# Kernel optimization log

Measured on AMD Instinct MI355X. Metric: run time of the kernel, lower is better.

## Reference

```python
import jax, jax.numpy as jnp
import numpy as np

C = 3.0
K = 1.0 / C
SQRT_K = K ** 0.5
GAMMA = 0.1
LAMBDA_STRUCTURE = 5.0
EPS = 1e-7
MIN_NORM = 1e-15
MAX_SQDIST = 50.0

N_NODES = 100000
HID = 64
E_POS = 250000
E_NEG = 250000
E_NONE = E_POS + E_NEG


def _arcosh(x):
    return jnp.log(x + jnp.sqrt(x * x - 1.0))


def hyp_sqdist(x, y):
    # Minkowski inner product: <x,y>_L = sum(x*y) - 2*x0*y0
    mdot = jnp.sum(x * y, axis=-1) - 2.0 * x[..., 0] * y[..., 0]
    theta = jnp.maximum(-mdot / K, 1.0 + EPS)
    return jnp.minimum(K * _arcosh(theta) ** 2, MAX_SQDIST)


def hyp_proj(x):
    # project onto hyperboloid: x0 = sqrt(K + ||x_1:||^2)
    y = x[..., 1:]
    x0 = jnp.sqrt(K + jnp.sum(y * y, axis=-1, keepdims=True))
    return jnp.concatenate([x0, y], axis=-1)


def hyp_expmap0(u):
    x = u[..., 1:]
    xn = jnp.maximum(jnp.sqrt(jnp.sum(x * x, axis=-1, keepdims=True)), MIN_NORM)
    theta = xn / SQRT_K
    res = jnp.concatenate([SQRT_K * jnp.cosh(theta), SQRT_K * jnp.sinh(theta) * x / xn], axis=-1)
    return hyp_proj(res)


def discriminate(z, ei, lin_w, lin_b):
    v = jnp.concatenate([z[ei[0]], z[ei[1]]], axis=-1)  # [E, 2*HID]
    return jax.nn.log_softmax(v @ lin_w.T + lin_b, axis=-1)


def info_net(v, y, w1, b1, w2, b2):
    # MINE-style critic: concat(edge_feature, label) -> Linear -> ReLU -> Linear -> scalar
    h = jnp.concatenate([v, y[:, None]], axis=-1)
    h = jax.nn.relu(h @ w1.T + b1)
    return (h @ w2.T + b2)[:, 0]


def setup_inputs():
    key = jax.random.key(0)
    ks = jax.random.split(key, 16)
    z = jax.random.normal(ks[0], (N_NODES, HID), dtype=jnp.float32)
    lin_w = 0.05 * jax.random.normal(ks[1], (3, 2 * HID), dtype=jnp.float32)
    lin_b = jnp.zeros((3,), dtype=jnp.float32)
    d_info = 2 * (HID + 1)
    info_w1 = 0.02 * jax.random.normal(ks[2], (d_info, d_info + 1), dtype=jnp.float32)
    info_b1 = jnp.zeros((d_info,), dtype=jnp.float32)
    info_w2 = 0.02 * jax.random.normal(ks[3], (1, d_info), dtype=jnp.float32)
    info_b2 = jnp.zeros((1,), dtype=jnp.float32)
    pos_edge_index = jax.random.randint(ks[4], (2, E_POS), 0, N_NODES)
    neg_edge_index = jax.random.randint(ks[5], (2, E_NEG), 0, N_NODES)
    none_edge_index = jax.random.randint(ks[6], (2, E_NONE), 0, N_NODES)
    none_edge_index2 = jax.random.randint(ks[7], (2, E_NONE), 0, N_NODES)
    pos_k = jax.random.randint(ks[8], (E_POS,), 0, N_NODES)
    neg_k = jax.random.randint(ks[9], (E_NEG,), 0, N_NODES)
    perm = jax.random.permutation(ks[10], E_POS + E_NEG + E_NONE)
    return dict(z=z, lin_w=lin_w, lin_b=lin_b, info_w1=info_w1, info_b1=info_b1,
                info_w2=info_w2, info_b2=info_b2, pos_edge_index=pos_edge_index,
                neg_edge_index=neg_edge_index, none_edge_index=none_edge_index,
                none_edge_index2=none_edge_index2, pos_k=pos_k, neg_k=neg_k, perm=perm)


def reference(z, lin_w, lin_b, info_w1, info_b1, info_w2, info_b2,
              pos_edge_index, neg_edge_index, none_edge_index,
              none_edge_index2, pos_k, neg_k, perm):
    # lift z onto the hyperboloid: proj(expmap0(proj_tan0([z0 | z])))
    vals = jnp.concatenate([z[:, :1], z], axis=1)      # [N, HID+1]
    u = vals.at[:, 0].set(0.0)                          # proj_tan0
    x = hyp_proj(hyp_expmap0(u))                        # [N, HID+1]

    # nll discriminator loss (class targets 0 / 1 / 2)
    nll = (jnp.mean(-discriminate(z, pos_edge_index, lin_w, lin_b)[:, 0])
           + jnp.mean(-discriminate(z, neg_edge_index, lin_w, lin_b)[:, 1])
           + jnp.mean(-discriminate(z, none_edge_index, lin_w, lin_b)[:, 2])) / 3.0

    # structured triplet losses on the hyperboloid
    i, j = pos_edge_index[0], pos_edge_index[1]
    l1 = jnp.mean(jnp.maximum(hyp_sqdist(x[i], x[j]) - hyp_sqdist(x[i], x[pos_k]), 0.0))
    i, j = neg_edge_index[0], neg_edge_index[1]
    l2 = jnp.mean(jnp.maximum(hyp_sqdist(x[i], x[neg_k]) - hyp_sqdist(x[i], x[j]), 0.0))

    # mutual-information (MINE) term on hyperbolic embeddings
    idx = jnp.concatenate([pos_edge_index, neg_edge_index, none_edge_index2], axis=1)
    all_y = jnp.concatenate([
        jnp.zeros((pos_edge_index.shape[1],), jnp.float32),
        jnp.ones((neg_edge_index.shape[1],), jnp.float32),
        jnp.full((none_edge_index2.shape[1],), 2.0, jnp.float32)])
    value = jnp.concatenate([x[idx[0]], x[idx[1]]], axis=1)  # [E_all, 2*(HID+1)]
    info_pred = info_net(value, all_y, info_w1, info_b1, info_w2, info_b2)
    info_shuffle = info_net(value, all_y[perm], info_w1, info_b1, info_w2, info_b2)
    l3 = -(jnp.mean(info_pred) - jnp.log(jnp.mean(jnp.exp(info_shuffle))))

    return nll + LAMBDA_STRUCTURE * (l1 + l2) + GAMMA * l3
```

## Files before the change

kernel.cpp:

```cpp
#include <hip/hip_runtime.h>
#include <hip/hip_fp16.h>
#include <math.h>

#define NN    100000
#define EPOS  250000
#define ENEG  250000
#define ENON  500000
#define E3   1000000
#define EHALF 500000
#define NLSE  4096

#define NB_INFO   2816
#define NB_STRUCT 960
#define NB_NLL    320
#define NB_EDGES  (NB_INFO + NB_STRUCT + NB_NLL)

#define ACC_OFF 0
#define LSE_OFF 256
#define X0_OFF  66048
#define ZA_OFF  466176
#define ZB_OFF  2066176
#define WT_OFF  3666176
#define YF8_OFF 3722752
#define PT_OFF  10122752
#define QT_OFF  10322752
#define PM_OFF  10522752
#define QM_OFF  23322752

typedef __attribute__((ext_vector_type(8))) short bh8;
typedef __attribute__((ext_vector_type(4))) float f32x4;
typedef __attribute__((ext_vector_type(2))) float f32x2;


__device__ __forceinline__ unsigned short f2bf(float f) {
  unsigned u = __float_as_uint(f);
  unsigned r = (u + 0x7FFFu + ((u >> 16) & 1u)) >> 16;
  return (unsigned short)r;
}

#if __has_builtin(__builtin_amdgcn_cvt_pk_f32_bf8) && __has_builtin(__builtin_amdgcn_cvt_pk_bf8_f32)
#define HAVE_BF8 1
#endif

__device__ __forceinline__ void de4(unsigned v, float* o) {
#ifdef HAVE_BF8
  f32x2 lo = __builtin_amdgcn_cvt_pk_f32_bf8((int)v, false);
  f32x2 hi = __builtin_amdgcn_cvt_pk_f32_bf8((int)v, true);
  o[0] = lo[0]; o[1] = lo[1]; o[2] = hi[0]; o[3] = hi[1];
#else
  o[0] = __half2float(__ushort_as_half((unsigned short)((v & 0xFFu) << 8)));
  o[1] = __half2float(__ushort_as_half((unsigned short)(((v >> 8) & 0xFFu) << 8)));
  o[2] = __half2float(__ushort_as_half((unsigned short)(((v >> 16) & 0xFFu) << 8)));
  o[3] = __half2float(__ushort_as_half((unsigned short)((v >> 24) << 8)));
#endif
}

__device__ __forceinline__ unsigned pk2(float a, float b) {
  a = fminf(fmaxf(a, -57344.f), 57344.f);
  b = fminf(fmaxf(b, -57344.f), 57344.f);
#ifdef HAVE_BF8
  return (unsigned)__builtin_amdgcn_cvt_pk_bf8_f32(a, b, 0, false) & 0xFFFFu;
#else
  unsigned short ha = __half_as_ushort(__float2half(a));
  unsigned short hb = __half_as_ushort(__float2half(b));
  ha = (unsigned short)((ha + 0x7Fu + ((ha >> 8) & 1u)) >> 8);
  hb = (unsigned short)((hb + 0x7Fu + ((hb >> 8) & 1u)) >> 8);
  return (unsigned)ha | ((unsigned)hb << 8);
#endif
}

__device__ __forceinline__ void breduce2(double v0, double v1, double* g0, double* g1,
                                         double* rbuf) {
#pragma unroll
  for (int m = 32; m; m >>= 1) {
    v0 += __shfl_xor(v0, m, 64);
    v1 += __shfl_xor(v1, m, 64);
  }
  int l = threadIdx.x & 63, w = threadIdx.x >> 6;
  if (l == 0) { rbuf[2 * w] = v0; rbuf[2 * w + 1] = v1; }
  __syncthreads();
  if (threadIdx.x == 0) {
    int nw = blockDim.x >> 6;
    double s0 = 0.0, s1 = 0.0;
    for (int i = 0; i < nw; ++i) { s0 += rbuf[2 * i]; s1 += rbuf[2 * i + 1]; }
    atomicAdd(g0, s0);
    atomicAdd(g1, s1);
  }
}

__device__ __forceinline__ void lse_combine(double& m, double& s, double om, double os) {
  double M = fmax(m, om);
  double sn = 0.0;
  if (m > -INFINITY) sn += s * exp(m - M);
  if (om > -INFINITY) sn += os * exp(om - M);
  m = M;
  s = sn;
}

__device__ __forceinline__ void lse_block_reduce(double lm, double ls, double* out_pair,
                                                 double* rbuf) {
#pragma unroll
  for (int d = 32; d; d >>= 1) {
    double om = __shfl_xor(lm, d, 64);
    double os = __shfl_xor(ls, d, 64);
    lse_combine(lm, ls, om, os);
  }
  __syncthreads();
  int l = threadIdx.x & 63, w = threadIdx.x >> 6;
  if (l == 0) { rbuf[2 * w] = lm; rbuf[2 * w + 1] = ls; }
  __syncthreads();
  if (threadIdx.x == 0) {
    int nw = blockDim.x >> 6;
    double M = rbuf[0], S = rbuf[1];
    for (int i = 1; i < nw; ++i) lse_combine(M, S, rbuf[2 * i], rbuf[2 * i + 1]);
    out_pair[0] = M;
    out_pair[1] = S;
  }
}

__global__ __launch_bounds__(256) void k_init(const float* __restrict__ w1,
                                              double* __restrict__ acc,
                                              double* __restrict__ lse,
                                              unsigned short* __restrict__ wt) {
  int gid = blockIdx.x * 256 + threadIdx.x;
  if (gid < NLSE) { lse[2 * gid] = -INFINITY; lse[2 * gid + 1] = 0.0; }
  if (gid < 8) acc[gid] = 0.0;
  for (int u = threadIdx.x; u < 16 * 104; u += 256) {
    int c = 16 * blockIdx.x + u / 104;
    int k = u % 104;
    float val = 0.f;
    if (c < 130) {
      if (k < 64) val = w1[c * 131 + 1 + k];
      else if (k == 64) val = w1[c * 131];
    } else if (c >= 136 && c < 266) {
      int r = c - 136;
      if (k < 64) val = w1[r * 131 + 66 + k];
      else if (k == 64) val = w1[r * 131 + 65];
    }
    wt[(size_t)c * 104 + k] = f2bf(val);
  }
}

__global__ __launch_bounds__(128) void k_pre(
    const float* __restrict__ z, const float* __restrict__ lin_w,
    const unsigned short* __restrict__ wt,
    float* __restrict__ X0, unsigned char* __restrict__ YF8,
    float4* __restrict__ ZA4, float4* __restrict__ ZB4,
    unsigned char* __restrict__ Pm, unsigned char* __restrict__ Qm,
    unsigned char* __restrict__ PTb, unsigned char* __restrict__ QTb) {
  __shared__ float WL[384];
  __shared__ __align__(16) unsigned short YL[128 * 96];
  __shared__ __align__(16) unsigned char SB[2][16 * 304];
  for (int u = threadIdx.x; u < 384; u += 128) {
    int rr = u >> 6, d = u & 63;
    WL[u] = (rr < 3) ? lin_w[rr * 128 + d] : lin_w[(rr - 3) * 128 + 64 + d];
  }
  __syncthreads();
  const int base = blockIdx.x * 128;
  const int n = base + threadIdx.x;
  if (n < NN) {
    const float4* zr = (const float4*)(z + (size_t)n * 64);
    const float4* wl4 = (const float4*)WL;
    float4 zc[16];
    float zn2 = 0.f, d0 = 0.f, d1 = 0.f, d2 = 0.f, d3 = 0.f, d4 = 0.f, d5 = 0.f;
#pragma unroll
    for (int c = 0; c < 16; ++c) {
      float4 v = zr[c];
      zc[c] = v;
      zn2 += v.x * v.x + v.y * v.y + v.z * v.z + v.w * v.w;
      float4 w0 = wl4[c];
      float4 w1r = wl4[16 + c];
      float4 w2r = wl4[32 + c];
      float4 w3 = wl4[48 + c];
      float4 w4 = wl4[64 + c];
      float4 w5 = wl4[80 + c];
      d0 += v.x * w0.x + v.y * w0.y + v.z * w0.z + v.w * w0.w;
      d1 += v.x * w1r.x + v.y * w1r.y + v.z * w1r.z + v.w * w1r.w;
      d2 += v.x * w2r.x + v.y * w2r.y + v.z * w2r.z + v.w * w2r.w;
      d3 += v.x * w3.x + v.y * w3.y + v.z * w3.z + v.w * w3.w;
      d4 += v.x * w4.x + v.y * w4.y + v.z * w4.z + v.w * w4.w;
      d5 += v.x * w5.x + v.y * w5.y + v.z * w5.z + v.w * w5.w;
    }
    float zn = fmaxf(sqrtf(zn2), 1e-15f);
    float t = 1.7320508075688772f * zn;
    float e = __expf(t);
    float sh = 0.5f * (e - __frcp_rn(e));
    float fac = (t < 1e-4f) ? (1.f + t * t * 0.16666667f) : (sh / t);
    float yn2 = fac * fac * zn2;
    float x0 = sqrtf(0.33333333333333333f + yn2);
    X0[n] = x0;
    ZA4[n] = make_float4(d0, d1, d2, 0.f);
    ZB4[n] = make_float4(d3, d4, d5, 0.f);
    unsigned short* yrow = YL + threadIdx.x * 96;
    unsigned yu[16];
#pragma unroll
    for (int c = 0; c < 16; ++c) {
      float4 v = zc[c];
      ushort4 o;
      o.x = f2bf(fac * v.x); o.y = f2bf(fac * v.y);
      o.z = f2bf(fac * v.z); o.w = f2bf(fac * v.w);
      *(ushort4*)(yrow + 4 * c) = o;
      yu[c] = pk2(fac * v.x, fac * v.y) | (pk2(fac * v.z, fac * v.w) << 16);
    }
    ushort4 xx; xx.x = f2bf(x0); xx.y = 0; xx.z = 0; xx.w = 0;
    *(ushort4*)(yrow + 64) = xx;
    ushort4 zz; zz.x = 0; zz.y = 0; zz.z = 0; zz.w = 0;
#pragma unroll
    for (int c = 17; c < 24; ++c) *(ushort4*)(yrow + 4 * c) = zz;
    uint4* y8 = (uint4*)(YF8 + (size_t)n * 64);
    y8[0] = make_uint4(yu[0], yu[1], yu[2], yu[3]);
    y8[1] = make_uint4(yu[4], yu[5], yu[6], yu[7]);
    y8[2] = make_uint4(yu[8], yu[9], yu[10], yu[11]);
    y8[3] = make_uint4(yu[12], yu[13], yu[14], yu[15]);
  }
  __syncthreads();
  const int l = threadIdx.x & 63;
  const int w = threadIdx.x >> 6;
  const int col = l & 15, kq = l >> 4;
  unsigned char* sb = SB[w];
  const int ntiles = min(8, (NN - base) >> 4);
  for (int t = w; t < ntiles; t += 2) {
    const unsigned short* yr = YL + (t * 16 + col) * 96 + kq * 8;
    bh8 y0 = *(const bh8*)(yr);
    bh8 y1 = *(const bh8*)(yr + 32);
    bh8 y2 = *(const bh8*)(yr + 64);
#pragma unroll
    for (int nt = 0; nt < 17; ++nt) {
      const unsigned short* wr = wt + (size_t)(nt * 16 + col) * 104 + kq * 8;
      bh8 b0 = *(const bh8*)(wr);
      bh8 b1 = *(const bh8*)(wr + 32);
      bh8 b2 = *(const bh8*)(wr + 64);
      f32x4 a4 = {0.f, 0.f, 0.f, 0.f};
      a4 = __builtin_amdgcn_mfma_f32_16x16x32_bf16(b0, y0, a4, 0, 0, 0);
      a4 = __builtin_amdgcn_mfma_f32_16x16x32_bf16(b1, y1, a4, 0, 0, 0);
      a4 = __builtin_amdgcn_mfma_f32_16x16x32_bf16(b2, y2, a4, 0, 0, 0);
      int ob = nt * 16 + kq * 4;
      unsigned u = pk2(a4[0], a4[1]) | (pk2(a4[2], a4[3]) << 16);
      unsigned char* row = sb + col * 304;
      if (nt < 8) {
        *(unsigned*)(row + ob) = u;
      } else if (nt == 8) {
        if (kq == 0) *(unsigned short*)(row + 256) = (unsigned short)(u & 0xFFFFu);
        else if (kq >= 2) *(unsigned*)(row + 128 + (ob - 136)) = u;
      } else if (nt < 16) {
        *(unsigned*)(row + 128 + (ob - 136)) = u;
      } else {
        if (kq < 2) *(unsigned*)(row + 128 + (ob - 136)) = u;
        else if (kq == 2) *(unsigned short*)(row + 258) = (unsigned short)(u & 0xFFFFu);
      }
    }
    const size_t gb = (size_t)(base + t * 16);
#pragma unroll
    for (int r = 0; r < 2; ++r) {
      int idx = r * 64 + l;
      int node = idx >> 3, part = idx & 7;
      uint4 vp = *(const uint4*)(sb + node * 304 + part * 16);
      *(uint4*)(Pm + (gb + node) * 128 + part * 16) = vp;
      uint4 vq = *(const uint4*)(sb + node * 304 + 128 + part * 16);
      *(uint4*)(Qm + (gb + node) * 128 + part * 16) = vq;
    }
    if (l < 16) {
      *(unsigned short*)(PTb + (gb + l) * 2) = *(const unsigned short*)(sb + l * 304 + 256);
      *(unsigned short*)(QTb + (gb + l) * 2) = *(const unsigned short*)(sb + l * 304 + 258);
    }
  }
}

__device__ __forceinline__ float hsq(float mdot) {
  float th = fmaxf(-3.f * mdot, 1.f + 1e-7f);
  float ach = __logf(th + sqrtf(th * th - 1.f));
  return fminf(ach * ach * (1.f / 3.f), 50.f);
}

__global__ __launch_bounds__(256) void k_edges(
    const int* __restrict__ p0, const int* __restrict__ p1,
    const int* __restrict__ n0, const int* __restrict__ n1,
    const int* __restrict__ o0, const int* __restrict__ o1,
    const int* __restrict__ q0, const int* __restrict__ q1,
    const int* __restrict__ pk, const int* __restrict__ nk,
    const int* __restrict__ perm,
    const unsigned char* __restrict__ Pm, const unsigned char* __restrict__ Qm,
    const unsigned short* __restrict__ PT, const unsigned short* __restrict__ QT,
    const unsigned char* __restrict__ YF8, const float* __restrict__ X0,
    const float4* __restrict__ ZA4, const float4* __restrict__ ZB4,
    const float* __restrict__ lin_b,
    const float* __restrict__ w1, const float* __restrict__ b1v,
    const float* __restrict__ w2v,
    double* __restrict__ acc, double* __restrict__ lse) {
  __shared__ double rbuf[8];
  __shared__ double rbuf2[8];

  if (blockIdx.x < NB_INFO) {
    const int s8 = threadIdx.x & 7;
    float byr[16], wyr[16], w2r[16];
#pragma unroll
    for (int q = 0; q < 16; ++q) {
      int k = 16 * s8 + q;
      byr[q] = b1v[k];
      wyr[q] = w1[k * 131 + 130];
      w2r[q] = w2v[k];
    }
    const float byt0 = b1v[128], byt1 = b1v[129];
    const float wyt0 = w1[128 * 131 + 130], wyt1 = w1[129 * 131 + 130];
    const float w2t0 = w2v[128], w2t1 = w2v[129];
    int g = (blockIdx.x * 256 + threadIdx.x) >> 3;
    const int gs = (NB_INFO * 256) >> 3;
    float s1f = 0.f, lm = -INFINITY, lsum = 0.f;

    int yAp_c = 0, yAs_c = 0, yBs_c = 0;
    uint4 PA_c = {}, QA_c = {}, PB_c = {}, QB_c = {};
    unsigned ptA_c = 0, qtA_c = 0, ptB_c = 0, qtB_c = 0;

#define FETCH_A(E, YPI, YSI, P4, Q4, PT_, QT_)                                          \
  {                                                                                     \
    int i, j;                                                                           \
    if ((E) < EPOS) { i = p0[E]; j = p1[E]; YPI = 0; }                                  \
    else { int t_ = (E) - EPOS; i = n0[t_]; j = n1[t_]; YPI = 1; }                      \
    int p_ = perm[E];                                                                   \
    YSI = (p_ < EPOS) ? 0 : ((p_ < EPOS + ENEG) ? 1 : 2);                               \
    P4 = *(const uint4*)(Pm + (size_t)i * 128 + 16 * s8);                               \
    Q4 = *(const uint4*)(Qm + (size_t)j * 128 + 16 * s8);                               \
    if (s8 == 0) { PT_ = PT[i]; QT_ = QT[j]; }                                          \
  }
#define FETCH_B(E, YSI, P4, Q4, PT_, QT_)                                               \
  {                                                                                     \
    int i = q0[E], j = q1[E];                                                           \
    int p_ = perm[(E) + EHALF];                                                         \
    YSI = (p_ < EPOS) ? 0 : ((p_ < EPOS + ENEG) ? 1 : 2);                               \
    P4 = *(const uint4*)(Pm + (size_t)i * 128 + 16 * s8);                               \
    Q4 = *(const uint4*)(Qm + (size_t)j * 128 + 16 * s8);                               \
    if (s8 == 0) { PT_ = PT[i]; QT_ = QT[j]; }                                          \
  }
#define INFO_COMPUTE(YPF, YSF, P4, Q4, PT_, QT_)                                        \
  {                                                                                     \
    float pv[16], qv[16];                                                               \
    de4(P4.x, pv); de4(P4.y, pv + 4); de4(P4.z, pv + 8); de4(P4.w, pv + 12);            \
    de4(Q4.x, qv); de4(Q4.y, qv + 4); de4(Q4.z, qv + 8); de4(Q4.w, qv + 12);            \
    float sp = 0.f, ss = 0.f;                                                           \
    _Pragma("unroll") for (int q = 0; q < 16; ++q) {                                    \
      float t_ = pv[q] + qv[q] + byr[q];                                                \
      sp = fmaf(fmaxf(fmaf(YPF, wyr[q], t_), 0.f), w2r[q], sp);                         \
      ss = fmaf(fmaxf(fmaf(YSF, wyr[q], t_), 0.f), w2r[q], ss);                         \
    }                                                                                   \
    if (s8 == 0) {                                                                      \
      float tp[4], tq[4];                                                               \
      de4(PT_, tp); de4(QT_, tq);                                                       \
      float t0 = tp[0] + tq[0] + byt0;                                                  \
      float t1 = tp[1] + tq[1] + byt1;                                                  \
      sp += fmaxf(fmaf(YPF, wyt0, t0), 0.f) * w2t0 + fmaxf(fmaf(YPF, wyt1, t1), 0.f) * w2t1; \
      ss += fmaxf(fmaf(YSF, wyt0, t0), 0.f) * w2t0 + fmaxf(fmaf(YSF, wyt1, t1), 0.f) * w2t1; \
    }                                                                                   \
    _Pragma("unroll") for (int m_ = 4; m_; m_ >>= 1) {                                  \
      sp += __shfl_xor(sp, m_, 64);                                                     \
      ss += __shfl_xor(ss, m_, 64);                                                     \
    }                                                                                   \
    if (s8 == 0) {                                                                      \
      s1f += sp;                                                                        \
      float nm = fmaxf(lm, ss);                                                         \
      lsum = lsum * __expf(lm - nm) + __expf(ss - nm);                                  \
      lm = nm;                                                                          \
    }                                                                                   \
  }

    int e = g;
    if (e < EHALF) {
      FETCH_A(e, yAp_c, yAs_c, PA_c, QA_c, ptA_c, qtA_c);
      FETCH_B(e, yBs_c, PB_c, QB_c, ptB_c, qtB_c);
    }
    while (e < EHALF) {
      int e2 = e + gs;
      int yAp_n = 0, yAs_n = 0, yBs_n = 0;
      uint4 PA_n = {}, QA_n = {}, PB_n = {}, QB_n = {};
      unsigned ptA_n = 0, qtA_n = 0, ptB_n = 0, qtB_n = 0;
      if (e2 < EHALF) {
        FETCH_A(e2, yAp_n, yAs_n, PA_n, QA_n, ptA_n, qtA_n);
        FETCH_B(e2, yBs_n, PB_n, QB_n, ptB_n, qtB_n);
      }
      INFO_COMPUTE((float)yAp_c, (float)yAs_c, PA_c, QA_c, ptA_c, qtA_c);
      INFO_COMPUTE(2.f, (float)yBs_c, PB_c, QB_c, ptB_c, qtB_c);
      e = e2;
      yAp_c = yAp_n; yAs_c = yAs_n; yBs_c = yBs_n;
      PA_c = PA_n; QA_c = QA_n; PB_c = PB_n; QB_c = QB_n;
      ptA_c = ptA_n; qtA_c = qtA_n; ptB_c = ptB_n; qtB_c = qtB_n;
    }
    breduce2((double)s1f, 0.0, acc + 3, acc + 6, rbuf);
    double lmd = (lsum > 0.f) ? (double)lm : -(double)INFINITY;
    lse_block_reduce(lmd, (double)lsum, lse + 2 * blockIdx.x, rbuf2);

  } else if (blockIdx.x < NB_INFO + NB_STRUCT) {
    const int st = threadIdx.x & 7;
    int g = ((blockIdx.x - NB_INFO) * 256 + threadIdx.x) >> 3;
    const int gs = (NB_STRUCT * 256) >> 3;
    float s1f = 0.f, s2f = 0.f;

    bool pos_c = false;
    uint2 yi_c = {}, yj_c = {}, yk_c = {};
    float xi_c = 0.f, xj_c = 0.f, xk_c = 0.f;

#define ST_FETCH(E, POS, YI, YJ, YK, XI, XJ, XK)                       \
  {                                                                    \
    int i, j, kk;                                                      \
    POS = (E) < EPOS;                                                  \
    if (POS) { i = p0[E]; j = p1[E]; kk = pk[E]; }                     \
    else { int t = (E) - EPOS; i = n0[t]; j = n1[t]; kk = nk[t]; }     \
    YI = *(const uint2*)(YF8 + (size_t)i * 64 + 8 * st);               \
    YJ = *(const uint2*)(YF8 + (size_t)j * 64 + 8 * st);               \
    YK = *(const uint2*)(YF8 + (size_t)kk * 64 + 8 * st);              \
    if (st == 0) { XI = X0[i]; XJ = X0[j]; XK = X0[kk]; }              \
  }

    int e = g;
    if (e < EPOS + ENEG) ST_FETCH(e, pos_c, yi_c, yj_c, yk_c, xi_c, xj_c, xk_c);
    while (e < EPOS + ENEG) {
      int e2 = e + gs;
      bool pos_n = false;
      uint2 yi_n = {}, yj_n = {}, yk_n = {};
      float xi_n = 0.f, xj_n = 0.f, xk_n = 0.f;
      if (e2 < EPOS + ENEG) ST_FETCH(e2, pos_n, yi_n, yj_n, yk_n, xi_n, xj_n, xk_n);
      float ai[8], aj[8], ak[8];
      de4(yi_c.x, ai); de4(yi_c.y, ai + 4);
      de4(yj_c.x, aj); de4(yj_c.y, aj + 4);
      de4(yk_c.x, ak); de4(yk_c.y, ak + 4);
      float dij = 0.f, dik = 0.f;
#pragma unroll
      for (int q = 0; q < 8; ++q) {
        dij = fmaf(ai[q], aj[q], dij);
        dik = fmaf(ai[q], ak[q], dik);
      }
#pragma unroll
      for (int m = 4; m; m >>= 1) {
        dij += __shfl_xor(dij, m, 64);
        dik += __shfl_xor(dik, m, 64);
      }
      if (st == 0) {
        float sij = hsq(dij - xi_c * xj_c);
        float sik = hsq(dik - xi_c * xk_c);
        if (pos_c) s1f += fmaxf(sij - sik, 0.f);
        else s2f += fmaxf(sik - sij, 0.f);
      }
      e = e2;
      pos_c = pos_n; yi_c = yi_n; yj_c = yj_n; yk_c = yk_n;
      xi_c = xi_n; xj_c = xj_n; xk_c = xk_n;
    }
    breduce2((double)s1f, (double)s2f, acc + 1, acc + 2, rbuf);

  } else {
    const float c0 = lin_b[0], c1 = lin_b[1], c2 = lin_b[2];
    const float wp = 1.f / (3.f * EPOS), wn = 1.f / (3.f * ENEG), wo = 1.f / (3.f * ENON);
    double s = 0.0;
    int t0 = (blockIdx.x - NB_INFO - NB_STRUCT) * 256 + threadIdx.x;
    for (int e = t0; e < E3; e += NB_NLL * 256) {
      int i, j, tgt;
      float wgt;
      if (e < EPOS) { i = p0[e]; j = p1[e]; tgt = 0; wgt = wp; }
      else if (e < EPOS + ENEG) { int t = e - EPOS; i = n0[t]; j = n1[t]; tgt = 1; wgt = wn; }
      else { int t = e - EPOS - ENEG; i = o0[t]; j = o1[t]; tgt = 2; wgt = wo; }
      float4 a = ZA4[i], b = ZB4[j];
      float l0 = a.x + b.x + c0, l1 = a.y + b.y + c1, l2 = a.z + b.z + c2;
      float mx = fmaxf(l0, fmaxf(l1, l2));
      float lsev = mx + __logf(__expf(l0 - mx) + __expf(l1 - mx) + __expf(l2 - mx));
      float lt = (tgt == 0) ? l0 : ((tgt == 1) ? l1 : l2);
      s += (double)((lsev - lt) * wgt);
    }
    breduce2(s, 0.0, acc + 0, acc + 5, rbuf);
  }
}

__global__ void k_final(const double* __restrict__ acc, const double* __restrict__ lse,
                        float* __restrict__ out) {
  __shared__ double rb[8];
  double lm = -INFINITY, ls = 0.0;
  for (int i = threadIdx.x; i < NLSE; i += blockDim.x)
    lse_combine(lm, ls, lse[2 * i], lse[2 * i + 1]);
#pragma unroll
  for (int d = 32; d; d >>= 1) {
    double om = __shfl_xor(lm, d, 64);
    double os = __shfl_xor(ls, d, 64);
    lse_combine(lm, ls, om, os);
  }
  int l = threadIdx.x & 63, w = threadIdx.x >> 6;
  if (l == 0) { rb[2 * w] = lm; rb[2 * w + 1] = ls; }
  __syncthreads();
  if (threadIdx.x == 0) {
    double M = rb[0], S = rb[1];
    int nw = blockDim.x >> 6;
    for (int i = 1; i < nw; ++i) lse_combine(M, S, rb[2 * i], rb[2 * i + 1]);
    double logmean = M + log(S) - log((double)E3);
    double nll = acc[0];
    double l1 = acc[1] / (double)EPOS;
    double l2 = acc[2] / (double)ENEG;
    double s1m = acc[3] / (double)E3;
    double l3 = -(s1m - logmean);
    out[0] = (float)(nll + 5.0 * (l1 + l2) + 0.1 * l3);
  }
}

extern "C" void kernel_launch(void* const* d_in, const int* in_sizes, int n_in,
                              void* d_out, int out_size, void* d_ws, size_t ws_size,
                              hipStream_t stream) {
  const float* z     = (const float*)d_in[0];
  const float* lin_w = (const float*)d_in[1];
  const float* lin_b = (const float*)d_in[2];
  const float* w1    = (const float*)d_in[3];
  const float* b1v   = (const float*)d_in[4];
  const float* w2v   = (const float*)d_in[5];
  const int* pos  = (const int*)d_in[7];
  const int* neg  = (const int*)d_in[8];
  const int* non  = (const int*)d_in[9];
  const int* non2 = (const int*)d_in[10];
  const int* posk = (const int*)d_in[11];
  const int* negk = (const int*)d_in[12];
  const int* perm = (const int*)d_in[13];

  char* ws = (char*)d_ws;
  double* acc = (double*)(ws + ACC_OFF);
  double* lse = (double*)(ws + LSE_OFF);
  float* X0   = (float*)(ws + X0_OFF);
  float4* ZA4 = (float4*)(ws + ZA_OFF);
  float4* ZB4 = (float4*)(ws + ZB_OFF);
  unsigned short* WT  = (unsigned short*)(ws + WT_OFF);
  unsigned char* YF8  = (unsigned char*)(ws + YF8_OFF);
  unsigned char* PTb  = (unsigned char*)(ws + PT_OFF);
  unsigned char* QTb  = (unsigned char*)(ws + QT_OFF);
  unsigned char* PM   = (unsigned char*)(ws + PM_OFF);
  unsigned char* QM   = (unsigned char*)(ws + QM_OFF);

  hipLaunchKernelGGL(k_init, dim3(17), dim3(256), 0, stream, w1, acc, lse, WT);
  hipLaunchKernelGGL(k_pre, dim3((NN + 127) / 128), dim3(128), 0, stream,
                     z, lin_w, WT, X0, YF8, ZA4, ZB4, PM, QM, PTb, QTb);
  hipLaunchKernelGGL(k_edges, dim3(NB_EDGES), dim3(256), 0, stream,
                     pos, pos + EPOS, neg, neg + ENEG, non, non + ENON,
                     non2, non2 + ENON, posk, negk, perm,
                     PM, QM, (const unsigned short*)PTb, (const unsigned short*)QTb,
                     YF8, X0, ZA4, ZB4, lin_b, w1, b1v, w2v, acc, lse);
  hipLaunchKernelGGL(k_final, dim3(1), dim3(256), 0, stream, acc, lse, (float*)d_out);
}
```

Before: 274.3 us.

## Split node precompute into two kernels and flatten info loop with two-deep prefetch

The fused node-preprocessing kernel is split in two. The first kernel computes the hyperbolic projection and writes bf16 rows to a new global buffer. The second kernel stages the MFMA weight table in shared memory once per block and loops persistently over 16-node tiles, where before every tile re-read the weights from global memory. The info-net edge loop now walks all 1M edges in one flat index space with a two-deep software prefetch instead of processing two halves per iteration. In exchange this adds a ~19MB intermediate write and read plus an extra kernel launch.

```diff
diff --git a/kernel.cpp b/kernel.cpp
--- a/kernel.cpp
+++ b/kernel.cpp
@@ -7,7 +7,6 @@
 #define ENEG  250000
 #define ENON  500000
 #define E3   1000000
-#define EHALF 500000
 #define NLSE  4096
 
 #define NB_INFO   2816
@@ -21,11 +20,12 @@
 #define ZA_OFF  466176
 #define ZB_OFF  2066176
 #define WT_OFF  3666176
-#define YF8_OFF 3722752
-#define PT_OFF  10122752
-#define QT_OFF  10322752
-#define PM_OFF  10522752
-#define QM_OFF  23322752
+#define YBF_OFF 3722752
+#define YF8_OFF 22922752
+#define PT_OFF  29322752
+#define QT_OFF  29522752
+#define PM_OFF  29722752
+#define QM_OFF  42522752
 
 typedef __attribute__((ext_vector_type(8))) short bh8;
 typedef __attribute__((ext_vector_type(4))) float f32x4;
@@ -141,92 +141,99 @@
   }
 }
 
-__global__ __launch_bounds__(128) void k_pre(
+__global__ __launch_bounds__(256) void k_pre1(
     const float* __restrict__ z, const float* __restrict__ lin_w,
-    const unsigned short* __restrict__ wt,
-    float* __restrict__ X0, unsigned char* __restrict__ YF8,
-    float4* __restrict__ ZA4, float4* __restrict__ ZB4,
+    float* __restrict__ X0, unsigned short* __restrict__ YBF,
+    unsigned char* __restrict__ YF8,
+    float4* __restrict__ ZA4, float4* __restrict__ ZB4) {
+  __shared__ float WL[384];
+  for (int u = threadIdx.x; u < 384; u += 256) {
+    int rr = u >> 6, d = u & 63;
+    WL[u] = (rr < 3) ? lin_w[rr * 128 + d] : lin_w[(rr - 3) * 128 + 64 + d];
+  }
+  __syncthreads();
+  int n = blockIdx.x * 256 + threadIdx.x;
+  if (n >= NN) return;
+  const float4* zr = (const float4*)(z + (size_t)n * 64);
+  const float4* wl4 = (const float4*)WL;
+  float4 zc[16];
+  float zn2 = 0.f, d0 = 0.f, d1 = 0.f, d2 = 0.f, d3 = 0.f, d4 = 0.f, d5 = 0.f;
+#pragma unroll
+  for (int c = 0; c < 16; ++c) {
+    float4 v = zr[c];
+    zc[c] = v;
+    zn2 += v.x * v.x + v.y * v.y + v.z * v.z + v.w * v.w;
+    float4 w0 = wl4[c];
+    float4 w1r = wl4[16 + c];
+    float4 w2r = wl4[32 + c];
+    float4 w3 = wl4[48 + c];
+    float4 w4 = wl4[64 + c];
+    float4 w5 = wl4[80 + c];
+    d0 += v.x * w0.x + v.y * w0.y + v.z * w0.z + v.w * w0.w;
+    d1 += v.x * w1r.x + v.y * w1r.y + v.z * w1r.z + v.w * w1r.w;
+    d2 += v.x * w2r.x + v.y * w2r.y + v.z * w2r.z + v.w * w2r.w;
+    d3 += v.x * w3.x + v.y * w3.y + v.z * w3.z + v.w * w3.w;
+    d4 += v.x * w4.x + v.y * w4.y + v.z * w4.z + v.w * w4.w;
+    d5 += v.x * w5.x + v.y * w5.y + v.z * w5.z + v.w * w5.w;
+  }
+  float zn = fmaxf(sqrtf(zn2), 1e-15f);
+  float t = 1.7320508075688772f * zn;
+  float e = __expf(t);
+  float sh = 0.5f * (e - __frcp_rn(e));
+  float fac = (t < 1e-4f) ? (1.f + t * t * 0.16666667f) : (sh / t);
+  float yn2 = fac * fac * zn2;
+  float x0 = sqrtf(0.33333333333333333f + yn2);
+  X0[n] = x0;
+  ZA4[n] = make_float4(d0, d1, d2, 0.f);
+  ZB4[n] = make_float4(d3, d4, d5, 0.f);
+  ushort4* yrow4 = (ushort4*)(YBF + (size_t)n * 96);
+  unsigned yu[16];
+#pragma unroll
+  for (int c = 0; c < 16; ++c) {
+    float4 v = zc[c];
+    ushort4 o;
+    o.x = f2bf(fac * v.x); o.y = f2bf(fac * v.y);
+    o.z = f2bf(fac * v.z); o.w = f2bf(fac * v.w);
+    yrow4[c] = o;
+    yu[c] = pk2(fac * v.x, fac * v.y) | (pk2(fac * v.z, fac * v.w) << 16);
+  }
+  ushort4 xx; xx.x = f2bf(x0); xx.y = 0; xx.z = 0; xx.w = 0;
+  yrow4[16] = xx;
+  ushort4 zz; zz.x = 0; zz.y = 0; zz.z = 0; zz.w = 0;
+#pragma unroll
+  for (int c = 17; c < 24; ++c) yrow4[c] = zz;
+  uint4* y8 = (uint4*)(YF8 + (size_t)n * 64);
+  y8[0] = make_uint4(yu[0], yu[1], yu[2], yu[3]);
+  y8[1] = make_uint4(yu[4], yu[5], yu[6], yu[7]);
+  y8[2] = make_uint4(yu[8], yu[9], yu[10], yu[11]);
+  y8[3] = make_uint4(yu[12], yu[13], yu[14], yu[15]);
+}
+
+__global__ __launch_bounds__(256) void k_pre2(
+    const unsigned short* __restrict__ ybf, const unsigned short* __restrict__ wt,
     unsigned char* __restrict__ Pm, unsigned char* __restrict__ Qm,
     unsigned char* __restrict__ PTb, unsigned char* __restrict__ QTb) {
-  __shared__ float WL[384];
-  __shared__ __align__(16) unsigned short YL[128 * 96];
-  __shared__ __align__(16) unsigned char SB[2][16 * 304];
-  for (int u = threadIdx.x; u < 384; u += 128) {
-    int rr = u >> 6, d = u & 63;
-    WL[u] = (rr < 3) ? lin_w[rr * 128 + d] : lin_w[(rr - 3) * 128 + 64 + d];
-  }
-  __syncthreads();
-  const int base = blockIdx.x * 128;
-  const int n = base + threadIdx.x;
-  if (n < NN) {
-    const float4* zr = (const float4*)(z + (size_t)n * 64);
-    const float4* wl4 = (const float4*)WL;
-    float4 zc[16];
-    float zn2 = 0.f, d0 = 0.f, d1 = 0.f, d2 = 0.f, d3 = 0.f, d4 = 0.f, d5 = 0.f;
-#pragma unroll
-    for (int c = 0; c < 16; ++c) {
-      float4 v = zr[c];
-      zc[c] = v;
-      zn2 += v.x * v.x + v.y * v.y + v.z * v.z + v.w * v.w;
-      float4 w0 = wl4[c];
-      float4 w1r = wl4[16 + c];
-      float4 w2r = wl4[32 + c];
-      float4 w3 = wl4[48 + c];
-      float4 w4 = wl4[64 + c];
-      float4 w5 = wl4[80 + c];
-      d0 += v.x * w0.x + v.y * w0.y + v.z * w0.z + v.w * w0.w;
-      d1 += v.x * w1r.x + v.y * w1r.y + v.z * w1r.z + v.w * w1r.w;
-      d2 += v.x * w2r.x + v.y * w2r.y + v.z * w2r.z + v.w * w2r.w;
-      d3 += v.x * w3.x + v.y * w3.y + v.z * w3.z + v.w * w3.w;
-      d4 += v.x * w4.x + v.y * w4.y + v.z * w4.z + v.w * w4.w;
-      d5 += v.x * w5.x + v.y * w5.y + v.z * w5.z + v.w * w5.w;
-    }
-    float zn = fmaxf(sqrtf(zn2), 1e-15f);
-    float t = 1.7320508075688772f * zn;
-    float e = __expf(t);
-    float sh = 0.5f * (e - __frcp_rn(e));
-    float fac = (t < 1e-4f) ? (1.f + t * t * 0.16666667f) : (sh / t);
-    float yn2 = fac * fac * zn2;
-    float x0 = sqrtf(0.33333333333333333f + yn2);
-    X0[n] = x0;
-    ZA4[n] = make_float4(d0, d1, d2, 0.f);
-    ZB4[n] = make_float4(d3, d4, d5, 0.f);
-    unsigned short* yrow = YL + threadIdx.x * 96;
-    unsigned yu[16];
-#pragma unroll
-    for (int c = 0; c < 16; ++c) {
-      float4 v = zc[c];
-      ushort4 o;
-      o.x = f2bf(fac * v.x); o.y = f2bf(fac * v.y);
-      o.z = f2bf(fac * v.z); o.w = f2bf(fac * v.w);
-      *(ushort4*)(yrow + 4 * c) = o;
-      yu[c] = pk2(fac * v.x, fac * v.y) | (pk2(fac * v.z, fac * v.w) << 16);
-    }
-    ushort4 xx; xx.x = f2bf(x0); xx.y = 0; xx.z = 0; xx.w = 0;
-    *(ushort4*)(yrow + 64) = xx;
-    ushort4 zz; zz.x = 0; zz.y = 0; zz.z = 0; zz.w = 0;
-#pragma unroll
-    for (int c = 17; c < 24; ++c) *(ushort4*)(yrow + 4 * c) = zz;
-    uint4* y8 = (uint4*)(YF8 + (size_t)n * 64);
-    y8[0] = make_uint4(yu[0], yu[1], yu[2], yu[3]);
-    y8[1] = make_uint4(yu[4], yu[5], yu[6], yu[7]);
-    y8[2] = make_uint4(yu[8], yu[9], yu[10], yu[11]);
-    y8[3] = make_uint4(yu[12], yu[13], yu[14], yu[15]);
+  __shared__ __align__(16) short WTs[28288];
+  __shared__ __align__(16) unsigned char SB[4][16 * 304];
+  {
+    float4* d = (float4*)WTs;
+    const float4* s = (const float4*)wt;
+    for (int u = threadIdx.x; u < 3536; u += 256) d[u] = s[u];
   }
   __syncthreads();
   const int l = threadIdx.x & 63;
   const int w = threadIdx.x >> 6;
   const int col = l & 15, kq = l >> 4;
   unsigned char* sb = SB[w];
-  const int ntiles = min(8, (NN - base) >> 4);
-  for (int t = w; t < ntiles; t += 2) {
-    const unsigned short* yr = YL + (t * 16 + col) * 96 + kq * 8;
+  for (int tile = blockIdx.x * 4 + w; tile < NN / 16; tile += 2048) {
+    const int nb = tile * 16;
+    const unsigned short* yr = ybf + (size_t)(nb + col) * 96 + kq * 8;
     bh8 y0 = *(const bh8*)(yr);
     bh8 y1 = *(const bh8*)(yr + 32);
     bh8 y2 = *(const bh8*)(yr + 64);
 #pragma unroll
     for (int nt = 0; nt < 17; ++nt) {
-      const unsigned short* wr = wt + (size_t)(nt * 16 + col) * 104 + kq * 8;
+      const short* wr = WTs + (nt * 16 + col) * 104 + kq * 8;
       bh8 b0 = *(const bh8*)(wr);
       bh8 b1 = *(const bh8*)(wr + 32);
       bh8 b2 = *(const bh8*)(wr + 64);
@@ -249,7 +256,7 @@
         else if (kq == 2) *(unsigned short*)(row + 258) = (unsigned short)(u & 0xFFFFu);
       }
     }
-    const size_t gb = (size_t)(base + t * 16);
+    const size_t gb = (size_t)nb;
 #pragma unroll
     for (int r = 0; r < 2; ++r) {
       int idx = r * 64 + l;
@@ -307,29 +314,21 @@
     const int gs = (NB_INFO * 256) >> 3;
     float s1f = 0.f, lm = -INFINITY, lsum = 0.f;
 
-    int yAp_c = 0, yAs_c = 0, yBs_c = 0;
-    uint4 PA_c = {}, QA_c = {}, PB_c = {}, QB_c = {};
-    unsigned ptA_c = 0, qtA_c = 0, ptB_c = 0, qtB_c = 0;
-
-#define FETCH_A(E, YPI, YSI, P4, Q4, PT_, QT_)                                          \
-  {                                                                                     \
-    int i, j;                                                                           \
-    if ((E) < EPOS) { i = p0[E]; j = p1[E]; YPI = 0; }                                  \
-    else { int t_ = (E) - EPOS; i = n0[t_]; j = n1[t_]; YPI = 1; }                      \
-    int p_ = perm[E];                                                                   \
-    YSI = (p_ < EPOS) ? 0 : ((p_ < EPOS + ENEG) ? 1 : 2);                               \
-    P4 = *(const uint4*)(Pm + (size_t)i * 128 + 16 * s8);                               \
-    Q4 = *(const uint4*)(Qm + (size_t)j * 128 + 16 * s8);                               \
-    if (s8 == 0) { PT_ = PT[i]; QT_ = QT[j]; }                                          \
-  }
-#define FETCH_B(E, YSI, P4, Q4, PT_, QT_)                                               \
-  {                                                                                     \
-    int i = q0[E], j = q1[E];                                                           \
-    int p_ = perm[(E) + EHALF];                                                         \
-    YSI = (p_ < EPOS) ? 0 : ((p_ < EPOS + ENEG) ? 1 : 2);                               \
-    P4 = *(const uint4*)(Pm + (size_t)i * 128 + 16 * s8);                               \
-    Q4 = *(const uint4*)(Qm + (size_t)j * 128 + 16 * s8);                               \
-    if (s8 == 0) { PT_ = PT[i]; QT_ = QT[j]; }                                          \
+    int ypi_c = 0, ysi_c = 0, ypi_1 = 0, ysi_1 = 0, ypi_2 = 0, ysi_2 = 0;
+    uint4 P_c = {}, Q_c = {}, P_1 = {}, Q_1 = {}, P_2 = {}, Q_2 = {};
+    unsigned pt_c = 0, qt_c = 0, pt_1 = 0, qt_1 = 0, pt_2 = 0, qt_2 = 0;
+
+#define INFO_FETCH(E, YPI, YSI, P4, Q4, PT_, QT_)                                        \
+  {                                                                                      \
+    int i, j;                                                                            \
+    if ((E) < EPOS) { i = p0[E]; j = p1[E]; YPI = 0; }                                   \
+    else if ((E) < EPOS + ENEG) { int t_ = (E) - EPOS; i = n0[t_]; j = n1[t_]; YPI = 1; }\
+    else { int t_ = (E) - EPOS - ENEG; i = q0[t_]; j = q1[t_]; YPI = 2; }                \
+    int p_ = perm[E];                                                                    \
+    YSI = (p_ < EPOS) ? 0 : ((p_ < EPOS + ENEG) ? 1 : 2);                                \
+    P4 = *(const uint4*)(Pm + (size_t)i * 128 + 16 * s8);                                \
+    Q4 = *(const uint4*)(Qm + (size_t)j * 128 + 16 * s8);                                \
+    if (s8 == 0) { PT_ = PT[i]; QT_ = QT[j]; }                                           \
   }
 #define INFO_COMPUTE(YPF, YSF, P4, Q4, PT_, QT_)                                        \
   {                                                                                     \
@@ -362,27 +361,20 @@
     }                                                                                   \
   }
 
-    int e = g;
-    if (e < EHALF) {
-      FETCH_A(e, yAp_c, yAs_c, PA_c, QA_c, ptA_c, qtA_c);
-      FETCH_B(e, yBs_c, PB_c, QB_c, ptB_c, qtB_c);
-    }
-    while (e < EHALF) {
-      int e2 = e + gs;
-      int yAp_n = 0, yAs_n = 0, yBs_n = 0;
-      uint4 PA_n = {}, QA_n = {}, PB_n = {}, QB_n = {};
-      unsigned ptA_n = 0, qtA_n = 0, ptB_n = 0, qtB_n = 0;
-      if (e2 < EHALF) {
-        FETCH_A(e2, yAp_n, yAs_n, PA_n, QA_n, ptA_n, qtA_n);
-        FETCH_B(e2, yBs_n, PB_n, QB_n, ptB_n, qtB_n);
-      }
-      INFO_COMPUTE((float)yAp_c, (float)yAs_c, PA_c, QA_c, ptA_c, qtA_c);
-      INFO_COMPUTE(2.f, (float)yBs_c, PB_c, QB_c, ptB_c, qtB_c);
-      e = e2;
-      yAp_c = yAp_n; yAs_c = yAs_n; yBs_c = yBs_n;
-      PA_c = PA_n; QA_c = QA_n; PB_c = PB_n; QB_c = QB_n;
-      ptA_c = ptA_n; qtA_c = qtA_n; ptB_c = ptB_n; qtB_c = qtB_n;
-    }
+    int e0 = g, e1 = g + gs, e2 = g + 2 * gs;
+    if (e0 < E3) INFO_FETCH(e0, ypi_c, ysi_c, P_c, Q_c, pt_c, qt_c);
+    if (e1 < E3) INFO_FETCH(e1, ypi_1, ysi_1, P_1, Q_1, pt_1, qt_1);
+    while (e0 < E3) {
+      int ypi_n = 0, ysi_n = 0;
+      uint4 P_n = {}, Q_n = {};
+      unsigned pt_n = 0, qt_n = 0;
+      if (e2 < E3) INFO_FETCH(e2, ypi_n, ysi_n, P_n, Q_n, pt_n, qt_n);
+      INFO_COMPUTE((float)ypi_c, (float)ysi_c, P_c, Q_c, pt_c, qt_c);
+      ypi_c = ypi_1; ysi_c = ysi_1; P_c = P_1; Q_c = Q_1; pt_c = pt_1; qt_c = qt_1;
+      ypi_1 = ypi_n; ysi_1 = ysi_n; P_1 = P_n; Q_1 = Q_n; pt_1 = pt_n; qt_1 = qt_n;
+      e0 = e1; e1 = e2; e2 += gs;
+    }
+    (void)ypi_2; (void)ysi_2; (void)P_2; (void)Q_2; (void)pt_2; (void)qt_2;
     breduce2((double)s1f, 0.0, acc + 3, acc + 6, rbuf);
     double lmd = (lsum > 0.f) ? (double)lm : -(double)INFINITY;
     lse_block_reduce(lmd, (double)lsum, lse + 2 * blockIdx.x, rbuf2);
@@ -519,6 +511,7 @@
   float4* ZA4 = (float4*)(ws + ZA_OFF);
   float4* ZB4 = (float4*)(ws + ZB_OFF);
   unsigned short* WT  = (unsigned short*)(ws + WT_OFF);
+  unsigned short* YBF = (unsigned short*)(ws + YBF_OFF);
   unsigned char* YF8  = (unsigned char*)(ws + YF8_OFF);
   unsigned char* PTb  = (unsigned char*)(ws + PT_OFF);
   unsigned char* QTb  = (unsigned char*)(ws + QT_OFF);
@@ -526,8 +519,9 @@
   unsigned char* QM   = (unsigned char*)(ws + QM_OFF);
 
   hipLaunchKernelGGL(k_init, dim3(17), dim3(256), 0, stream, w1, acc, lse, WT);
-  hipLaunchKernelGGL(k_pre, dim3((NN + 127) / 128), dim3(128), 0, stream,
-                     z, lin_w, WT, X0, YF8, ZA4, ZB4, PM, QM, PTb, QTb);
+  hipLaunchKernelGGL(k_pre1, dim3((NN + 255) / 256), dim3(256), 0, stream,
+                     z, lin_w, X0, YBF, YF8, ZA4, ZB4);
+  hipLaunchKernelGGL(k_pre2, dim3(512), dim3(256), 0, stream, YBF, WT, PM, QM, PTb, QTb);
   hipLaunchKernelGGL(k_edges, dim3(NB_EDGES), dim3(256), 0, stream,
                      pos, pos + EPOS, neg, neg + ENEG, non, non + ENON,
                      non2, non2 + ENON, posk, negk, perm,
```

Result: slower. 280.0 us (+2.1%).
